# Optimization experiments

Hardware: AMD Instinct MI355X
Metric: run time of the kernel (lower is better)

## Reference

```python
import jax, jax.numpy as jnp
import numpy as np

C = 1024          # channels
RED = 16          # reduction
RC = C // RED     # 64 bottleneck channels
BZ, NUM_PROPS = 4, 256
BP = BZ * NUM_PROPS


def setup_inputs() -> dict:
    key = jax.random.key(0)
    ks = jax.random.split(key, 10)
    x_props = jax.random.normal(ks[0], (BP, C, 7, 7), dtype=jnp.float32)
    x_query = jax.random.normal(ks[1], (BZ, C, 8, 8), dtype=jnp.float32)
    s_conv = 1.0 / np.sqrt(C)   # kaiming-uniform-ish for conv1d 1x1 (fan_in=C)
    s_mlp = 1.0 / np.sqrt(RC)   # Linear fan_in = RC
    pc_w = jax.random.uniform(ks[2], (RC, C), minval=-s_conv, maxval=s_conv)
    pc_b = jax.random.uniform(ks[3], (RC,), minval=-s_conv, maxval=s_conv)
    qc_w = jax.random.uniform(ks[4], (RC, C), minval=-s_conv, maxval=s_conv)
    qc_b = jax.random.uniform(ks[5], (RC,), minval=-s_conv, maxval=s_conv)
    pm_w = jax.random.uniform(ks[6], (C, RC), minval=-s_mlp, maxval=s_mlp)
    pm_b = jax.random.uniform(ks[7], (C,), minval=-s_mlp, maxval=s_mlp)
    qm_w = jax.random.uniform(ks[8], (C, RC), minval=-s_mlp, maxval=s_mlp)
    qm_b = jax.random.uniform(ks[9], (C,), minval=-s_mlp, maxval=s_mlp)
    return {"x_props": x_props, "x_query": x_query,
            "pc_w": pc_w, "pc_b": pc_b, "qc_w": qc_w, "qc_b": qc_b,
            "pm_w": pm_w, "pm_b": pm_b, "qm_w": qm_w, "qm_b": qm_b}


def reference(x_props, x_query, pc_w, pc_b, qc_w, qc_b, pm_w, pm_b, qm_w, qm_b):
    bp, c, hp, wp = x_props.shape
    bz, _, hq, wq = x_query.shape
    n = bp // bz
    L = hp * wp
    # bilinear resize (half-pixel centers == torch align_corners=False)
    r_query = jax.image.resize(x_query, (bz, c, hp, wp), method='bilinear')
    # 1x1 conv bottlenecks (conv1d over flattened spatial dim)
    q_feat = jnp.einsum('rc,bcl->brl', qc_w, r_query.reshape(bz, c, L)) + qc_b[None, :, None]   # [bz, RC, L]
    p_feat = jnp.einsum('rc,bcl->brl', pc_w, x_props.reshape(bp, c, L)) + pc_b[None, :, None]   # [bp, RC, L]
    # similarity contracts spatial dim; query feature shared across props of same image
    p_feat_g = p_feat.reshape(bz, n, -1, L)
    sim = jnp.einsum('bnrl,bsl->bnrs', p_feat_g, q_feat)                                        # [bz, n, RC, RC]
    p_rel = sim.mean(axis=3).reshape(bp, -1)                                                    # [bp, RC]
    q_rel = sim.mean(axis=2).reshape(bp, -1)                                                    # [bp, RC]
    # channel-gate MLPs
    p_att = jax.nn.sigmoid(p_rel @ pm_w.T + pm_b)                                               # [bp, C]
    q_att = jax.nn.sigmoid(q_rel @ qm_w.T + qm_b)                                               # [bp, C]
    # co-excitation
    f_props = x_props * p_att[:, :, None, None]
    xq_rep = jnp.broadcast_to(x_query[:, None], (bz, n, c, hq, wq)).reshape(bp, c, hq, wq)
    f_query = xq_rep * q_att[:, :, None, None]
    return f_props, f_query, p_att.reshape(bp, c, 1, 1)
```

## Files before the change

### kernel.cpp

```cpp
#include <hip/hip_runtime.h>


typedef float v4f __attribute__((ext_vector_type(4)));

#define WQBAR  0
#define WSUMQ  256
#define WPCBW  320
#define WPCBB  1344
#define WQF    1408
#define WPMBF  14336
#define WQMBF  47104
#define WQATT  79872

#define OUT_FP 0
#define OUT_FQ 51380224
#define OUT_PA 118489088

__device__ __forceinline__ float sigmoidf(float v) {
    return 1.0f / (1.0f + __expf(-v));
}
__device__ __forceinline__ unsigned short bf16_rne(float x) {
    unsigned u = __float_as_uint(x);
    return (unsigned short)((u + 0x7FFFu + ((u >> 16) & 1u)) >> 16);
}
__device__ __forceinline__ unsigned div49(unsigned e) {
    return __umulhi(e, 2804876602u) >> 5;
}

__global__ __launch_bounds__(1024) void k_qprep(
    const float* __restrict__ xq, const float* __restrict__ qc_w,
    const float* __restrict__ qc_b, float* __restrict__ ws)
{
    __shared__ float rq[1024];
    __shared__ float qf_s[64];
    const int blk = blockIdx.x;
    const int b = blk / 49, l = blk - b * 49;
    const int t = threadIdx.x, wave = t >> 6, lane = t & 63;
    const int i = l / 7, j = l - i * 7;
    float fi = (2 * i + 1) * (1.0f / 14.0f);
    float fj = (2 * j + 1) * (1.0f / 14.0f);
    float wi0 = (1.0f - 0.875f * fi) * (1.0f / 1.125f); float wi1 = 1.0f - wi0;
    float wj0 = (1.0f - 0.875f * fj) * (1.0f / 1.125f); float wj1 = 1.0f - wj0;
    const float* X = xq + ((size_t)(b * 1024 + t) << 6);
    rq[t] = wi0 * (wj0 * X[i * 8 + j]       + wj1 * X[i * 8 + j + 1])
          + wi1 * (wj0 * X[(i + 1) * 8 + j] + wj1 * X[(i + 1) * 8 + j + 1]);
    __syncthreads();
    #pragma unroll
    for (int ii = 0; ii < 4; ++ii) {
        int s = wave * 4 + ii;
        const float* wr = qc_w + s * 1024;
        float part = 0.0f;
        #pragma unroll
        for (int k = 0; k < 16; ++k) part += wr[k * 64 + lane] * rq[k * 64 + lane];
        #pragma unroll
        for (int off = 32; off; off >>= 1) part += __shfl_down(part, off, 64);
        if (lane == 0) {
            float val = part + qc_b[s];
            ws[WQF + b * 3136 + s * 49 + l] = val;
            qf_s[s] = val;
        }
    }
    __syncthreads();
    if (t == 0) {
        float s = 0.0f;
        #pragma unroll
        for (int k = 0; k < 64; ++k) s += qf_s[k];
        ws[WQBAR + b * 49 + l] = s * (1.0f / 64.0f);
    }
}

__global__ __launch_bounds__(1024) void k_prep(
    const float* __restrict__ pc_w, const float* __restrict__ pc_b,
    const float* __restrict__ pm_w, const float* __restrict__ qm_w,
    float* __restrict__ ws)
{
    int t = threadIdx.x;
    if (blockIdx.x == 0) {
        float s = 0.0f;
        for (int r = 0; r < 64; ++r) s += pc_w[r * 1024 + t];
        ws[WPCBW + t] = s * (1.0f / 64.0f);
        if (t == 0) {
            float sb = 0.0f;
            for (int r = 0; r < 64; ++r) sb += pc_b[r];
            ws[WPCBB] = sb * (1.0f / 64.0f);
        }
        if (t < 4) {
            float sq = 0.0f;
            for (int l = 0; l < 49; ++l) sq += ws[WQBAR + t * 49 + l];
            ws[WSUMQ + t] = sq;
        }
    } else {
        int idx = (blockIdx.x - 1) * 1024 + t;
        int r = (idx & 65535) >> 10, c = idx & 1023;
        float w = (idx < 65536) ? pm_w[c * 64 + r] : qm_w[c * 64 + r];
        unsigned short* dst = (unsigned short*)(ws + (idx < 65536 ? WPMBF : WQMBF));
        dst[idx & 65535] = bf16_rne(w);
    }
}

__global__ __launch_bounds__(512) void k_red(
    const float* __restrict__ x,
    const float* __restrict__ pc_w, const float* __restrict__ pc_b,
    const float* __restrict__ pm_b, const float* __restrict__ qm_b,
    float* __restrict__ ws, float* __restrict__ patt_out)
{
    __shared__ float xs[12544];
    __shared__ float y_s[1024];
    __shared__ float pcb_s[1024];
    __shared__ float qbar_s[49];
    __shared__ float pbar_part[4][49];
    __shared__ float pbar_s[49];
    __shared__ float prel_s[64];
    __shared__ float qrel_s[64];

    const int t = threadIdx.x, wave = t >> 6, lane = t & 63;
    const int p = blockIdx.x, b = p >> 8;

    if (t < 49) qbar_s[t] = ws[WQBAR + b * 49 + t];
    for (int k = t; k < 1024; k += 512) pcb_s[k] = ws[WPCBW + k];
    const float sumqbar = ws[WSUMQ + b];
    const float pcbarb  = ws[WPCBB];

    const float4* xp4 = (const float4*)(x + (size_t)p * 50176);
    float pbar_acc = 0.0f;

    for (int ch = 0; ch < 4; ++ch) {
        __syncthreads();
        const float4* src = xp4 + ch * 3136;
        float4* xs4 = (float4*)xs;
        for (int k = t; k < 3136; k += 512) xs4[k] = src[k];
        __syncthreads();
        if (wave < 4) {
            int c = wave * 64 + lane;
            const float* row = xs + c * 49;
            float acc = 0.0f;
            #pragma unroll
            for (int l = 0; l < 49; ++l) acc += row[l] * qbar_s[l];
            y_s[ch * 256 + c] = acc;
        } else if (lane < 49) {
            int cw = (wave - 4) * 64;
            const float* base = xs + cw * 49 + lane;
            const float* pw = pcb_s + ch * 256 + cw;
            float a = 0.0f;
            #pragma unroll
            for (int c = 0; c < 64; ++c) a += pw[c] * base[c * 49];
            pbar_acc += a;
        }
    }
    if (wave >= 4 && lane < 49) pbar_part[wave - 4][lane] = pbar_acc;
    __syncthreads();
    if (t < 49)
        pbar_s[t] = pbar_part[0][t] + pbar_part[1][t] + pbar_part[2][t] + pbar_part[3][t] + pcbarb;
    __syncthreads();

    #pragma unroll
    for (int i = 0; i < 8; ++i) {
        int r = wave * 8 + i;
        const float* wr = pc_w + r * 1024;
        float part = 0.0f;
        #pragma unroll
        for (int k = 0; k < 16; ++k) part += wr[k * 64 + lane] * y_s[k * 64 + lane];
        #pragma unroll
        for (int off = 32; off; off >>= 1) part += __shfl_down(part, off, 64);
        if (lane == 0) prel_s[r] = part + pc_b[r] * sumqbar;
    }
    if (t < 64) {
        const float* qfr = ws + WQF + (b * 3136 + t * 49);
        float a = 0.0f;
        #pragma unroll
        for (int l = 0; l < 49; ++l) a += pbar_s[l] * qfr[l];
        qrel_s[t] = a;
    }
    __syncthreads();

    {
        int col = t & 255;
        const unsigned* wbf = (const unsigned*)(ws + (t < 256 ? WPMBF : WQMBF));
        const float* rel = (t < 256) ? prel_s : qrel_s;
        float4 a = {0, 0, 0, 0};
        #pragma unroll
        for (int r = 0; r < 64; ++r) {
            unsigned w01 = wbf[r * 512 + 2 * col];
            unsigned w23 = wbf[r * 512 + 2 * col + 1];
            float rv = rel[r];
            a.x += __uint_as_float(w01 << 16) * rv;
            a.y += __uint_as_float(w01 & 0xFFFF0000u) * rv;
            a.z += __uint_as_float(w23 << 16) * rv;
            a.w += __uint_as_float(w23 & 0xFFFF0000u) * rv;
        }
        const float4* bias4 = (const float4*)((t < 256) ? pm_b : qm_b);
        float4 bb = bias4[col];
        float4 o;
        o.x = sigmoidf(a.x + bb.x); o.y = sigmoidf(a.y + bb.y);
        o.z = sigmoidf(a.z + bb.z); o.w = sigmoidf(a.w + bb.w);
        if (t < 256) ((float4*)patt_out)[p * 256 + col] = o;
        else         ((float4*)(ws + WQATT))[p * 256 + col] = o;
    }
}

#define NBLK_P 6144
#define NBLK_Q 2048
__global__ __launch_bounds__(256) void k_scale(
    const float* __restrict__ x, const float* __restrict__ xq,
    const float* __restrict__ patt, const float* __restrict__ qatt,
    float* __restrict__ fprops, float* __restrict__ fquery)
{
    if (blockIdx.x < NBLK_P) {
        const unsigned N4 = 12845056u;
        const unsigned stride = NBLK_P * 256;
        const v4f* s4 = (const v4f*)x;
        v4f* d4 = (v4f*)fprops;
        for (unsigned i = blockIdx.x * 256 + threadIdx.x; i < N4; i += stride) {
            unsigned e = i * 4u;
            unsigned q = div49(e);
            unsigned m = e - 49u * q;
            float a0 = patt[q];
            float a1 = patt[q + (m >= 46u)];
            v4f v = s4[i];
            v4f g;
            g.x = a0;
            g.y = (m >= 48u) ? a1 : a0;
            g.z = (m >= 47u) ? a1 : a0;
            g.w = (m >= 46u) ? a1 : a0;
            __builtin_nontemporal_store(v * g, d4 + i);
        }
    } else {
        const unsigned N4 = 16777216u;
        const unsigned stride = NBLK_Q * 256;
        const v4f* s4 = (const v4f*)xq;
        v4f* d4 = (v4f*)fquery;
        for (unsigned i = (blockIdx.x - NBLK_P) * 256 + threadIdx.x; i < N4; i += stride) {
            unsigned p = i >> 14;
            unsigned k = i & 16383u;
            float att = qatt[(p << 10) | (k >> 4)];
            v4f v = s4[(((size_t)(p >> 8)) << 14) | k];
            __builtin_nontemporal_store(v * att, d4 + i);
        }
    }
}

extern "C" void kernel_launch(void* const* d_in, const int* in_sizes, int n_in,
                              void* d_out, int out_size, void* d_ws, size_t ws_size,
                              hipStream_t stream) {
    const float* x_props = (const float*)d_in[0];
    const float* x_query = (const float*)d_in[1];
    const float* pc_w    = (const float*)d_in[2];
    const float* pc_b    = (const float*)d_in[3];
    const float* qc_w    = (const float*)d_in[4];
    const float* qc_b    = (const float*)d_in[5];
    const float* pm_w    = (const float*)d_in[6];
    const float* pm_b    = (const float*)d_in[7];
    const float* qm_w    = (const float*)d_in[8];
    const float* qm_b    = (const float*)d_in[9];
    float* out = (float*)d_out;
    float* ws  = (float*)d_ws;

    k_qprep<<<196, 1024, 0, stream>>>(x_query, qc_w, qc_b, ws);
    k_prep<<<129, 1024, 0, stream>>>(pc_w, pc_b, pm_w, qm_w, ws);
    k_red<<<1024, 512, 0, stream>>>(x_props, pc_w, pc_b, pm_b, qm_b, ws, out + OUT_PA);
    k_scale<<<NBLK_P + NBLK_Q, 256, 0, stream>>>(x_props, x_query, out + OUT_PA, ws + WQATT,
                                                 out + OUT_FP, out + OUT_FQ);
}
```

Before: 188.2 us.

## Merge prep kernels, shrink reduction block to 256 threads, unify scale loop

Folds the query-prep and weight-prep kernels into one launch, moving the sum of qbar into the reduction kernel so the cross-kernel dependency goes away. The reduction kernel now runs 256 threads with a half-size shared tile over 8 chunks, which lowers LDS use per block and may let more blocks fit per CU. Each thread in the gate MLP now computes both the p and q outputs. The scale kernel drops its fixed split between props and query blocks in favour of a single grid-stride loop over the combined range. The trade-offs are fewer threads per reduction block doing more serial work, and a per-element branch in the scale loop.

```diff
diff --git a/kernel.cpp b/kernel.cpp
--- a/kernel.cpp
+++ b/kernel.cpp
@@ -4,7 +4,6 @@
 typedef float v4f __attribute__((ext_vector_type(4)));
 
 #define WQBAR  0
-#define WSUMQ  256
 #define WPCBW  320
 #define WPCBB  1344
 #define WQF    1408
@@ -27,55 +26,50 @@
     return __umulhi(e, 2804876602u) >> 5;
 }
 
-__global__ __launch_bounds__(1024) void k_qprep(
+__global__ __launch_bounds__(1024) void k_prepall(
     const float* __restrict__ xq, const float* __restrict__ qc_w,
-    const float* __restrict__ qc_b, float* __restrict__ ws)
+    const float* __restrict__ qc_b, const float* __restrict__ pc_w,
+    const float* __restrict__ pc_b, const float* __restrict__ pm_w,
+    const float* __restrict__ qm_w, float* __restrict__ ws)
 {
-    __shared__ float rq[1024];
-    __shared__ float qf_s[64];
-    const int blk = blockIdx.x;
-    const int b = blk / 49, l = blk - b * 49;
-    const int t = threadIdx.x, wave = t >> 6, lane = t & 63;
-    const int i = l / 7, j = l - i * 7;
-    float fi = (2 * i + 1) * (1.0f / 14.0f);
-    float fj = (2 * j + 1) * (1.0f / 14.0f);
-    float wi0 = (1.0f - 0.875f * fi) * (1.0f / 1.125f); float wi1 = 1.0f - wi0;
-    float wj0 = (1.0f - 0.875f * fj) * (1.0f / 1.125f); float wj1 = 1.0f - wj0;
-    const float* X = xq + ((size_t)(b * 1024 + t) << 6);
-    rq[t] = wi0 * (wj0 * X[i * 8 + j]       + wj1 * X[i * 8 + j + 1])
-          + wi1 * (wj0 * X[(i + 1) * 8 + j] + wj1 * X[(i + 1) * 8 + j + 1]);
-    __syncthreads();
-    #pragma unroll
-    for (int ii = 0; ii < 4; ++ii) {
-        int s = wave * 4 + ii;
-        const float* wr = qc_w + s * 1024;
-        float part = 0.0f;
-        #pragma unroll
-        for (int k = 0; k < 16; ++k) part += wr[k * 64 + lane] * rq[k * 64 + lane];
-        #pragma unroll
-        for (int off = 32; off; off >>= 1) part += __shfl_down(part, off, 64);
-        if (lane == 0) {
-            float val = part + qc_b[s];
-            ws[WQF + b * 3136 + s * 49 + l] = val;
-            qf_s[s] = val;
-        }
-    }
-    __syncthreads();
-    if (t == 0) {
-        float s = 0.0f;
-        #pragma unroll
-        for (int k = 0; k < 64; ++k) s += qf_s[k];
-        ws[WQBAR + b * 49 + l] = s * (1.0f / 64.0f);
-    }
-}
-
-__global__ __launch_bounds__(1024) void k_prep(
-    const float* __restrict__ pc_w, const float* __restrict__ pc_b,
-    const float* __restrict__ pm_w, const float* __restrict__ qm_w,
-    float* __restrict__ ws)
-{
-    int t = threadIdx.x;
-    if (blockIdx.x == 0) {
+    const int blk = blockIdx.x, t = threadIdx.x;
+    if (blk < 196) {
+        __shared__ float rq[1024];
+        __shared__ float qf_s[64];
+        const int b = blk / 49, l = blk - b * 49;
+        const int wave = t >> 6, lane = t & 63;
+        const int i = l / 7, j = l - i * 7;
+        float fi = (2 * i + 1) * (1.0f / 14.0f);
+        float fj = (2 * j + 1) * (1.0f / 14.0f);
+        float wi0 = (1.0f - 0.875f * fi) * (1.0f / 1.125f); float wi1 = 1.0f - wi0;
+        float wj0 = (1.0f - 0.875f * fj) * (1.0f / 1.125f); float wj1 = 1.0f - wj0;
+        const float* X = xq + ((size_t)(b * 1024 + t) << 6);
+        rq[t] = wi0 * (wj0 * X[i * 8 + j]       + wj1 * X[i * 8 + j + 1])
+              + wi1 * (wj0 * X[(i + 1) * 8 + j] + wj1 * X[(i + 1) * 8 + j + 1]);
+        __syncthreads();
+        #pragma unroll
+        for (int ii = 0; ii < 4; ++ii) {
+            int s = wave * 4 + ii;
+            const float* wr = qc_w + s * 1024;
+            float part = 0.0f;
+            #pragma unroll
+            for (int k = 0; k < 16; ++k) part += wr[k * 64 + lane] * rq[k * 64 + lane];
+            #pragma unroll
+            for (int off = 32; off; off >>= 1) part += __shfl_down(part, off, 64);
+            if (lane == 0) {
+                float val = part + qc_b[s];
+                ws[WQF + b * 3136 + s * 49 + l] = val;
+                qf_s[s] = val;
+            }
+        }
+        __syncthreads();
+        if (t == 0) {
+            float s = 0.0f;
+            #pragma unroll
+            for (int k = 0; k < 64; ++k) s += qf_s[k];
+            ws[WQBAR + b * 49 + l] = s * (1.0f / 64.0f);
+        }
+    } else if (blk == 196) {
         float s = 0.0f;
         for (int r = 0; r < 64; ++r) s += pc_w[r * 1024 + t];
         ws[WPCBW + t] = s * (1.0f / 64.0f);
@@ -84,13 +78,8 @@
             for (int r = 0; r < 64; ++r) sb += pc_b[r];
             ws[WPCBB] = sb * (1.0f / 64.0f);
         }
-        if (t < 4) {
-            float sq = 0.0f;
-            for (int l = 0; l < 49; ++l) sq += ws[WQBAR + t * 49 + l];
-            ws[WSUMQ + t] = sq;
-        }
     } else {
-        int idx = (blockIdx.x - 1) * 1024 + t;
+        int idx = (blk - 197) * 1024 + t;
         int r = (idx & 65535) >> 10, c = idx & 1023;
         float w = (idx < 65536) ? pm_w[c * 64 + r] : qm_w[c * 64 + r];
         unsigned short* dst = (unsigned short*)(ws + (idx < 65536 ? WPMBF : WQMBF));
@@ -98,17 +87,18 @@
     }
 }
 
-__global__ __launch_bounds__(512) void k_red(
+__global__ __launch_bounds__(256) void k_red(
     const float* __restrict__ x,
     const float* __restrict__ pc_w, const float* __restrict__ pc_b,
     const float* __restrict__ pm_b, const float* __restrict__ qm_b,
     float* __restrict__ ws, float* __restrict__ patt_out)
 {
-    __shared__ float xs[12544];
+    __shared__ float xs[6272];
     __shared__ float y_s[1024];
     __shared__ float pcb_s[1024];
     __shared__ float qbar_s[49];
-    __shared__ float pbar_part[4][49];
+    __shared__ float sq_s;
+    __shared__ float pbar_part[2][49];
     __shared__ float pbar_s[49];
     __shared__ float prel_s[64];
     __shared__ float qrel_s[64];
@@ -117,45 +107,50 @@
     const int p = blockIdx.x, b = p >> 8;
 
     if (t < 49) qbar_s[t] = ws[WQBAR + b * 49 + t];
-    for (int k = t; k < 1024; k += 512) pcb_s[k] = ws[WPCBW + k];
-    const float sumqbar = ws[WSUMQ + b];
-    const float pcbarb  = ws[WPCBB];
+    for (int k = t; k < 1024; k += 256) pcb_s[k] = ws[WPCBW + k];
+    const float pcbarb = ws[WPCBB];
 
     const float4* xp4 = (const float4*)(x + (size_t)p * 50176);
     float pbar_acc = 0.0f;
 
-    for (int ch = 0; ch < 4; ++ch) {
-        __syncthreads();
-        const float4* src = xp4 + ch * 3136;
+    for (int ch = 0; ch < 8; ++ch) {
+        __syncthreads();
+        const float4* src = xp4 + ch * 1568;
         float4* xs4 = (float4*)xs;
-        for (int k = t; k < 3136; k += 512) xs4[k] = src[k];
-        __syncthreads();
-        if (wave < 4) {
+        for (int k = t; k < 1568; k += 256) xs4[k] = src[k];
+        __syncthreads();
+        if (ch == 0 && t == 0) {
+            float s = 0.0f;
+            #pragma unroll
+            for (int l = 0; l < 49; ++l) s += qbar_s[l];
+            sq_s = s;
+        }
+        if (wave < 2) {
             int c = wave * 64 + lane;
             const float* row = xs + c * 49;
             float acc = 0.0f;
             #pragma unroll
             for (int l = 0; l < 49; ++l) acc += row[l] * qbar_s[l];
-            y_s[ch * 256 + c] = acc;
+            y_s[ch * 128 + c] = acc;
         } else if (lane < 49) {
-            int cw = (wave - 4) * 64;
+            int cw = (wave - 2) * 64;
             const float* base = xs + cw * 49 + lane;
-            const float* pw = pcb_s + ch * 256 + cw;
+            const float* pw = pcb_s + ch * 128 + cw;
             float a = 0.0f;
             #pragma unroll
             for (int c = 0; c < 64; ++c) a += pw[c] * base[c * 49];
             pbar_acc += a;
         }
     }
-    if (wave >= 4 && lane < 49) pbar_part[wave - 4][lane] = pbar_acc;
+    if (wave >= 2 && lane < 49) pbar_part[wave - 2][lane] = pbar_acc;
     __syncthreads();
-    if (t < 49)
-        pbar_s[t] = pbar_part[0][t] + pbar_part[1][t] + pbar_part[2][t] + pbar_part[3][t] + pcbarb;
+    if (t < 49) pbar_s[t] = pbar_part[0][t] + pbar_part[1][t] + pcbarb;
     __syncthreads();
+    const float sumqbar = sq_s;
 
     #pragma unroll
-    for (int i = 0; i < 8; ++i) {
-        int r = wave * 8 + i;
+    for (int i = 0; i < 16; ++i) {
+        int r = wave * 16 + i;
         const float* wr = pc_w + r * 1024;
         float part = 0.0f;
         #pragma unroll
@@ -174,67 +169,66 @@
     __syncthreads();
 
     {
-        int col = t & 255;
-        const unsigned* wbf = (const unsigned*)(ws + (t < 256 ? WPMBF : WQMBF));
-        const float* rel = (t < 256) ? prel_s : qrel_s;
-        float4 a = {0, 0, 0, 0};
+        const unsigned* wp = (const unsigned*)(ws + WPMBF);
+        const unsigned* wq = (const unsigned*)(ws + WQMBF);
+        float4 ap = {0, 0, 0, 0}, aq = {0, 0, 0, 0};
         #pragma unroll
         for (int r = 0; r < 64; ++r) {
-            unsigned w01 = wbf[r * 512 + 2 * col];
-            unsigned w23 = wbf[r * 512 + 2 * col + 1];
-            float rv = rel[r];
-            a.x += __uint_as_float(w01 << 16) * rv;
-            a.y += __uint_as_float(w01 & 0xFFFF0000u) * rv;
-            a.z += __uint_as_float(w23 << 16) * rv;
-            a.w += __uint_as_float(w23 & 0xFFFF0000u) * rv;
-        }
-        const float4* bias4 = (const float4*)((t < 256) ? pm_b : qm_b);
-        float4 bb = bias4[col];
-        float4 o;
-        o.x = sigmoidf(a.x + bb.x); o.y = sigmoidf(a.y + bb.y);
-        o.z = sigmoidf(a.z + bb.z); o.w = sigmoidf(a.w + bb.w);
-        if (t < 256) ((float4*)patt_out)[p * 256 + col] = o;
-        else         ((float4*)(ws + WQATT))[p * 256 + col] = o;
-    }
-}
-
-#define NBLK_P 6144
-#define NBLK_Q 2048
+            float pr = prel_s[r], qr = qrel_s[r];
+            unsigned p01 = wp[r * 512 + 2 * t];
+            unsigned p23 = wp[r * 512 + 2 * t + 1];
+            ap.x += __uint_as_float(p01 << 16) * pr;
+            ap.y += __uint_as_float(p01 & 0xFFFF0000u) * pr;
+            ap.z += __uint_as_float(p23 << 16) * pr;
+            ap.w += __uint_as_float(p23 & 0xFFFF0000u) * pr;
+            unsigned q01 = wq[r * 512 + 2 * t];
+            unsigned q23 = wq[r * 512 + 2 * t + 1];
+            aq.x += __uint_as_float(q01 << 16) * qr;
+            aq.y += __uint_as_float(q01 & 0xFFFF0000u) * qr;
+            aq.z += __uint_as_float(q23 << 16) * qr;
+            aq.w += __uint_as_float(q23 & 0xFFFF0000u) * qr;
+        }
+        float4 pb = ((const float4*)pm_b)[t];
+        float4 qb = ((const float4*)qm_b)[t];
+        float4 po, qo;
+        po.x = sigmoidf(ap.x + pb.x); po.y = sigmoidf(ap.y + pb.y);
+        po.z = sigmoidf(ap.z + pb.z); po.w = sigmoidf(ap.w + pb.w);
+        qo.x = sigmoidf(aq.x + qb.x); qo.y = sigmoidf(aq.y + qb.y);
+        qo.z = sigmoidf(aq.z + qb.z); qo.w = sigmoidf(aq.w + qb.w);
+        ((float4*)patt_out)[p * 256 + t] = po;
+        ((float4*)(ws + WQATT))[p * 256 + t] = qo;
+    }
+}
+
 __global__ __launch_bounds__(256) void k_scale(
     const float* __restrict__ x, const float* __restrict__ xq,
     const float* __restrict__ patt, const float* __restrict__ qatt,
     float* __restrict__ fprops, float* __restrict__ fquery)
 {
-    if (blockIdx.x < NBLK_P) {
-        const unsigned N4 = 12845056u;
-        const unsigned stride = NBLK_P * 256;
-        const v4f* s4 = (const v4f*)x;
-        v4f* d4 = (v4f*)fprops;
-        for (unsigned i = blockIdx.x * 256 + threadIdx.x; i < N4; i += stride) {
+    const unsigned NP4 = 12845056u;
+    const unsigned NT4 = 29622272u;
+    const unsigned stride = gridDim.x * blockDim.x;
+    for (unsigned i = blockIdx.x * blockDim.x + threadIdx.x; i < NT4; i += stride) {
+        if (i < NP4) {
             unsigned e = i * 4u;
             unsigned q = div49(e);
             unsigned m = e - 49u * q;
             float a0 = patt[q];
             float a1 = patt[q + (m >= 46u)];
-            v4f v = s4[i];
+            v4f v = ((const v4f*)x)[i];
             v4f g;
             g.x = a0;
             g.y = (m >= 48u) ? a1 : a0;
             g.z = (m >= 47u) ? a1 : a0;
             g.w = (m >= 46u) ? a1 : a0;
-            __builtin_nontemporal_store(v * g, d4 + i);
-        }
-    } else {
-        const unsigned N4 = 16777216u;
-        const unsigned stride = NBLK_Q * 256;
-        const v4f* s4 = (const v4f*)xq;
-        v4f* d4 = (v4f*)fquery;
-        for (unsigned i = (blockIdx.x - NBLK_P) * 256 + threadIdx.x; i < N4; i += stride) {
-            unsigned p = i >> 14;
-            unsigned k = i & 16383u;
+            __builtin_nontemporal_store(v * g, (v4f*)fprops + i);
+        } else {
+            unsigned j = i - NP4;
+            unsigned p = j >> 14;
+            unsigned k = j & 16383u;
             float att = qatt[(p << 10) | (k >> 4)];
-            v4f v = s4[(((size_t)(p >> 8)) << 14) | k];
-            __builtin_nontemporal_store(v * att, d4 + i);
+            v4f v = ((const v4f*)xq)[(((size_t)(p >> 8)) << 14) | k];
+            __builtin_nontemporal_store(v * att, (v4f*)fquery + j);
         }
     }
 }
@@ -255,9 +249,8 @@
     float* out = (float*)d_out;
     float* ws  = (float*)d_ws;
 
-    k_qprep<<<196, 1024, 0, stream>>>(x_query, qc_w, qc_b, ws);
-    k_prep<<<129, 1024, 0, stream>>>(pc_w, pc_b, pm_w, qm_w, ws);
-    k_red<<<1024, 512, 0, stream>>>(x_props, pc_w, pc_b, pm_b, qm_b, ws, out + OUT_PA);
-    k_scale<<<NBLK_P + NBLK_Q, 256, 0, stream>>>(x_props, x_query, out + OUT_PA, ws + WQATT,
-                                                 out + OUT_FP, out + OUT_FQ);
-}
+    k_prepall<<<325, 1024, 0, stream>>>(x_query, qc_w, qc_b, pc_w, pc_b, pm_w, qm_w, ws);
+    k_red<<<1024, 256, 0, stream>>>(x_props, pc_w, pc_b, pm_b, qm_b, ws, out + OUT_PA);
+    k_scale<<<8192, 256, 0, stream>>>(x_props, x_query, out + OUT_PA, ws + WQATT,
+                                      out + OUT_FP, out + OUT_FQ);
+}
```

Result: faster. 172.9 us (-8.1%).
